# Performance work log

Measured on AMD Instinct MI355X. Metric: run time of the kernel, lower is better.

## Reference

```python
import jax, jax.numpy as jnp
import numpy as np

B, S, D = 4, 4096, 512
HEADS, NS, NEXT = 8, 32, 2048
HD = D // HEADS
SCALE = 1.0 / np.sqrt(HD)


def setup_inputs() -> dict:
    key = jax.random.key(0)
    ks = jax.random.split(key, 12)
    w_scale = 1.0 / np.sqrt(D)
    return {
        "sequence_tokens": jax.random.normal(ks[0], (B, S, D), jnp.float32),
        "sequence_mask": jnp.ones((B, S), dtype=bool),
        "ns_tokens": jax.random.normal(ks[1], (B, NS, D), jnp.float32),
        "ns_mask": jnp.ones((B, NS), dtype=bool),
        "next_sequence_length": NEXT,
        "Wq": jax.random.normal(ks[2], (D, D), jnp.float32) * w_scale,
        "Wk": jax.random.normal(ks[3], (D, D), jnp.float32) * w_scale,
        "Wv": jax.random.normal(ks[4], (D, D), jnp.float32) * w_scale,
        "ns_q_w": jax.random.normal(ks[5], (NS, D, D), jnp.float32) * w_scale,
        "ns_k_w": jax.random.normal(ks[6], (NS, D, D), jnp.float32) * w_scale,
        "ns_v_w": jax.random.normal(ks[7], (NS, D, D), jnp.float32) * w_scale,
        "Wo": jax.random.normal(ks[8], (D, D), jnp.float32) * w_scale,
    }


def reference(sequence_tokens, sequence_mask, ns_tokens, ns_mask,
              next_sequence_length, Wq, Wk, Wv, ns_q_w, ns_k_w, ns_v_w, Wo):
    b, s, d = sequence_tokens.shape
    ns = ns_tokens.shape[1]
    nxt = next_sequence_length

    seq_q = sequence_tokens[:, -nxt:]
    seq_q_mask = sequence_mask[:, -nxt:]

    # mixed projections: standard linear for seq tokens, per-position weights for NS tokens
    q = jnp.concatenate([seq_q @ Wq.T,
                         jnp.einsum('bnd,ndo->bno', ns_tokens, ns_q_w)], axis=1)
    k = jnp.concatenate([sequence_tokens @ Wk.T,
                         jnp.einsum('bnd,ndo->bno', ns_tokens, ns_k_w)], axis=1)
    v = jnp.concatenate([sequence_tokens @ Wv.T,
                         jnp.einsum('bnd,ndo->bno', ns_tokens, ns_v_w)], axis=1)

    def heads(x):  # [b, t, d] -> [b, h, t, hd]
        return x.reshape(b, -1, HEADS, HD).transpose(0, 2, 1, 3)
    q, k, v = heads(q), heads(k), heads(v)

    total = s + ns
    q_pos = jnp.concatenate([jnp.arange(s - nxt, s), jnp.arange(s, total)])
    k_pos = jnp.arange(total)
    causal = k_pos[None, :] <= q_pos[:, None]              # [Q, K]
    key_mask = jnp.concatenate([sequence_mask, ns_mask], axis=1)  # [b, K]

    logits = jnp.einsum('bhqd,bhkd->bhqk',
                        q.astype(jnp.float32), k.astype(jnp.float32)) * SCALE
    logits = jnp.where(causal[None, None], logits, -10000.0)
    logits = jnp.where(key_mask[:, None, None, :], logits, -10000.0)
    w = jax.nn.softmax(logits, axis=-1).astype(q.dtype)

    att = jnp.einsum('bhqk,bhkd->bhqd', w, v)
    att = att.transpose(0, 2, 1, 3).reshape(b, nxt + ns, d)
    att = att @ Wo.T

    seq_out = att[:, :nxt] * seq_q_mask[..., None].astype(att.dtype)
    ns_out = att[:, nxt:] * ns_mask[..., None].astype(att.dtype)
    return (seq_out, ns_out)
```

## Files before the change

### kernel.cpp

```cpp
#include <hip/hip_runtime.h>

#define NBATCH 4
#define SEQ    4096
#define DMODEL 512
#define NHEAD  8
#define HDIM   64
#define NSN    32
#define NXT    2048
#define QLEN   2080
#define KLEN   4128

using bf16x8 = __attribute__((ext_vector_type(8))) short;
using f32x4  = __attribute__((ext_vector_type(4))) float;

typedef __attribute__((address_space(1))) unsigned int gu32;
typedef __attribute__((address_space(3))) unsigned int lu32;

#define QSCALE 0.18033688f

__device__ __forceinline__ unsigned short f2bf(float f) {
  unsigned int u = __float_as_uint(f);
  u += 0x7FFF + ((u >> 16) & 1);
  return (unsigned short)(u >> 16);
}

__device__ __forceinline__ float bf2f(unsigned short u) {
  return __uint_as_float((unsigned int)u << 16);
}

__device__ __forceinline__ f32x4 mfma16(bf16x8 a, bf16x8 b, f32x4 c) {
  return __builtin_amdgcn_mfma_f32_16x16x32_bf16(a, b, c, 0, 0, 0);
}

__device__ __forceinline__ void gload_lds16(const void* g, void* lds_base) {
  __builtin_amdgcn_global_load_lds((const gu32*)g, (lu32*)lds_base, 16, 0, 0);
}

__device__ __forceinline__ unsigned int cvt_pk_bf16(float lo, float hi) {
  unsigned int r;
  asm("v_cvt_pk_bf16_f32 %0, %1, %2" : "=v"(r) : "v"(lo), "v"(hi));
  return r;
}

__global__ __launch_bounds__(256) void cvt_f32_bf16_v4(const float* __restrict__ src,
                                                       unsigned short* __restrict__ dst, int n4) {
  int i = blockIdx.x * 256 + threadIdx.x;
  if (i >= n4) return;
  float4 v = reinterpret_cast<const float4*>(src)[i];
  ushort4 r;
  r.x = f2bf(v.x); r.y = f2bf(v.y); r.z = f2bf(v.z); r.w = f2bf(v.w);
  reinterpret_cast<ushort4*>(dst)[i] = r;
}

__global__ __launch_bounds__(256) void cvt_w4(const float* __restrict__ a, const float* __restrict__ b,
                                              const float* __restrict__ c, const float* __restrict__ d,
                                              unsigned short* __restrict__ dst) {
  const float* s = blockIdx.y == 0 ? a : blockIdx.y == 1 ? b : blockIdx.y == 2 ? c : d;
  int i = blockIdx.x * 256 + threadIdx.x;
  float4 v = reinterpret_cast<const float4*>(s)[i];
  ushort4 r;
  r.x = f2bf(v.x); r.y = f2bf(v.y); r.z = f2bf(v.z); r.w = f2bf(v.w);
  reinterpret_cast<ushort4*>(dst)[(size_t)blockIdx.y * 65536 + i] = r;
}

__global__ __launch_bounds__(256) void proj_gemm(const unsigned short* __restrict__ X,
                                                 const unsigned short* __restrict__ W,
                                                 unsigned short* __restrict__ Out,
                                                 int rpb_shift, int row_off, int out_L, float scale) {
  __shared__ unsigned short As[64 * 32];
  __shared__ unsigned short Bs[128 * 32];
  const int tid = threadIdx.x;
  const int w = tid >> 6, l = tid & 63;
  const int lg = l >> 4, lr = l & 15;
  const int row0 = blockIdx.x * 64, col0 = blockIdx.y * 128;
  const int mask = (1 << rpb_shift) - 1;

  f32x4 acc[8];
#pragma unroll
  for (int n = 0; n < 8; ++n) acc[n] = (f32x4){0.f, 0.f, 0.f, 0.f};

  const int sra = tid >> 2;
  const int sca = (tid & 3) * 8;
  const int srb = w * 16 + (l >> 2);
  const int scb = (l & 3) * 8;
  const int gra = row0 + sra;
  const int xrow = ((gra >> rpb_shift) << 12) + row_off + (gra & mask);

  for (int k0 = 0; k0 < 512; k0 += 32) {
    const unsigned short* gpa = X + (size_t)xrow * 512 + k0 + sca;
    gload_lds16(gpa, (char*)As + w * 1024);
#pragma unroll
    for (int i = 0; i < 2; ++i) {
      const unsigned short* gpb = W + (size_t)(col0 + srb + i * 64) * 512 + k0 + scb;
      gload_lds16(gpb, (char*)Bs + i * 4096 + w * 1024);
    }
    __syncthreads();
    const bf16x8 avf = *(const bf16x8*)&As[(w * 16 + lr) * 32 + lg * 8];
#pragma unroll
    for (int n = 0; n < 8; ++n) {
      const bf16x8 bv = *(const bf16x8*)&Bs[(n * 16 + lr) * 32 + lg * 8];
      acc[n] = mfma16(avf, bv, acc[n]);
    }
    __syncthreads();
  }

  const int crow = row0 + w * 16 + lg * 4;
#pragma unroll
  for (int n = 0; n < 8; ++n) {
    const int ccol = col0 + n * 16 + lr;
    const int hh = ccol >> 6, dd = ccol & 63;
#pragma unroll
    for (int r = 0; r < 4; ++r) {
      int cr = crow + r;
      int bb = cr >> rpb_shift, ii = cr & mask;
      Out[(((size_t)bb * NHEAD + hh) * out_L + ii) * HDIM + dd] = f2bf(acc[n][r] * scale);
    }
  }
}

__global__ __launch_bounds__(256) void ns_proj(const float* __restrict__ nst,
                                               const float* __restrict__ Wnq, const float* __restrict__ Wnk,
                                               const float* __restrict__ Wnv,
                                               unsigned short* __restrict__ Qb, unsigned short* __restrict__ Kb,
                                               unsigned short* __restrict__ Vb) {
  const int oc = blockIdx.x, n = blockIdx.y, p = blockIdx.z;
  const float* W = p == 0 ? Wnq : p == 1 ? Wnk : Wnv;
  unsigned short* Out = p == 0 ? Qb : p == 1 ? Kb : Vb;
  const int out_L = p == 0 ? QLEN : KLEN;
  const int orow = p == 0 ? NXT + n : SEQ + n;
  const float scale = p == 0 ? QSCALE : 1.f;

  __shared__ float xs[NBATCH][DMODEL];
  __shared__ float red[NBATCH][128];
  const int tid = threadIdx.x;
  for (int idx = tid; idx < NBATCH * DMODEL; idx += 256)
    xs[idx >> 9][idx & 511] = nst[(size_t)((idx >> 9) * NSN + n) * DMODEL + (idx & 511)];
  __syncthreads();

  const int o = oc * 128 + (tid & 127);
  const int dh = tid >> 7;
  float a0 = 0.f, a1 = 0.f, a2 = 0.f, a3 = 0.f;
  const float* wp = W + (size_t)n * DMODEL * DMODEL + o;
#pragma unroll 8
  for (int d = dh * 256; d < dh * 256 + 256; ++d) {
    float wv = wp[(size_t)d * DMODEL];
    a0 += xs[0][d] * wv; a1 += xs[1][d] * wv; a2 += xs[2][d] * wv; a3 += xs[3][d] * wv;
  }
  if (dh == 1) { red[0][tid & 127] = a0; red[1][tid & 127] = a1; red[2][tid & 127] = a2; red[3][tid & 127] = a3; }
  __syncthreads();
  if (dh == 0) {
    a0 += red[0][tid & 127]; a1 += red[1][tid & 127]; a2 += red[2][tid & 127]; a3 += red[3][tid & 127];
    int hh = o >> 6, dd = o & 63;
    float v[4] = {a0, a1, a2, a3};
#pragma unroll
    for (int b = 0; b < NBATCH; ++b)
      Out[(((size_t)b * NHEAD + hh) * out_L + orow) * HDIM + dd] = f2bf(v[b] * scale);
  }
}

__global__ __launch_bounds__(256) void vtrans(const unsigned short* __restrict__ V,
                                              unsigned short* __restrict__ Vt) {
  __shared__ unsigned short t[64 * 64];
  const int tid = threadIdx.x;
  const int kv0 = blockIdx.x * 64, bh = blockIdx.y;
  const unsigned short* Vhp = V + (size_t)bh * KLEN * HDIM;
  unsigned short* Vtp = Vt + (size_t)bh * HDIM * KLEN;

#pragma unroll
  for (int i = 0; i < 2; ++i) {
    int c = i * 256 + tid;
    int row = c >> 3, c8 = c & 7;
    int kvg = kv0 + row; if (kvg > KLEN - 1) kvg = KLEN - 1;
    int4 v4 = *(const int4*)(Vhp + (size_t)kvg * HDIM + c8 * 8);
    *(int4*)&t[row * 64 + ((c8 ^ ((row >> 3) & 7)) * 8)] = v4;
  }
  __syncthreads();
#pragma unroll
  for (int i = 0; i < 2; ++i) {
    int c = i * 256 + tid;
    int d = c >> 3, k8 = c & 7;
    if (kv0 + k8 * 8 <= KLEN - 8) {
      unsigned int wd[4];
#pragma unroll
      for (int jj = 0; jj < 4; ++jj) {
        int ka = k8 * 8 + jj * 2, kb2 = ka + 1;
        unsigned int lo = t[ka  * 64 + (((d >> 3) ^ ((ka  >> 3) & 7)) * 8) + (d & 7)];
        unsigned int hi = t[kb2 * 64 + (((d >> 3) ^ ((kb2 >> 3) & 7)) * 8) + (d & 7)];
        wd[jj] = lo | (hi << 16);
      }
      int4 o; o.x = wd[0]; o.y = wd[1]; o.z = wd[2]; o.w = wd[3];
      *(int4*)(Vtp + (size_t)d * KLEN + kv0 + k8 * 8) = o;
    }
  }
}

__global__ __launch_bounds__(256) void attn_kernel(const unsigned short* __restrict__ Qb,
                                                   const unsigned short* __restrict__ Kb,
                                                   const unsigned short* __restrict__ Vtg,
                                                   unsigned short* __restrict__ PoA,
                                                   float* __restrict__ PlA,
                                                   unsigned short* __restrict__ PoB,
                                                   float* __restrict__ PlB) {
  __shared__ unsigned short Ks[64 * 64];
  __shared__ unsigned short Vs[64 * 64];

  const int tid = threadIdx.x;
  const int w = tid >> 6, l = tid & 63;
  const int lg = l >> 4, lr = l & 15;
  const bool geven = (l & 16) == 0;
  const int bx = (int)blockIdx.x;
  const int qb = 32 - bx / 3;
  const int sp = bx - 3 * (32 - qb);
  const int bh = (int)blockIdx.z * NHEAD + (int)blockIdx.y;
  const int q0 = qb * 64;
  const int base = NXT + q0;
  const int nkb = (base >> 6) + 1;
  const int t0 = (sp * nkb) / 3;
  const int t1 = ((sp + 1) * nkb) / 3;

  const unsigned short* Qh = Qb + (size_t)bh * QLEN * HDIM;
  const unsigned short* Kh = Kb + (size_t)bh * KLEN * HDIM;
  const unsigned short* Vh = Vtg + (size_t)bh * HDIM * KLEN;

  int qrow = q0 + w * 16 + lr; if (qrow > QLEN - 1) qrow = QLEN - 1;
  const bf16x8 qa0 = *(const bf16x8*)(Qh + (size_t)qrow * HDIM + lg * 8);
  const bf16x8 qa1 = *(const bf16x8*)(Qh + (size_t)qrow * HDIM + 32 + lg * 8);

  f32x4 acc[4];
#pragma unroll
  for (int n = 0; n < 4; ++n) acc[n] = (f32x4){0.f, 0.f, 0.f, 0.f};
  float lsum = 0.f;

  const bf16x8 ones = {(short)0x3F80, (short)0x3F80, (short)0x3F80, (short)0x3F80,
                       (short)0x3F80, (short)0x3F80, (short)0x3F80, (short)0x3F80};

  const int rloc = l >> 3;
  const int jsrc = ((l & 7) ^ rloc) * 8;

  for (int kb = t0; kb < t1; ++kb) {
    const int kv0 = kb * 64;
    if (kv0 + 64 <= KLEN) {
#pragma unroll
      for (int i = 0; i < 2; ++i) {
        const int r8 = (w * 2 + i) * 8;
        gload_lds16(Kh + (size_t)(kv0 + r8 + rloc) * HDIM + jsrc, &Ks[r8 * 64]);
        gload_lds16(Vh + (size_t)(r8 + rloc) * KLEN + kv0 + jsrc, &Vs[r8 * 64]);
      }
    } else {
#pragma unroll
      for (int i = 0; i < 2; ++i) {
        const int r8 = (w * 2 + i) * 8;
        int kr = kv0 + r8 + rloc; if (kr > KLEN - 1) kr = KLEN - 1;
        gload_lds16(Kh + (size_t)kr * HDIM + jsrc, &Ks[r8 * 64]);
        int vc = kv0 + jsrc; if (vc > KLEN - 8) vc = KLEN - 8;
        gload_lds16(Vh + (size_t)(r8 + rloc) * KLEN + vc, &Vs[r8 * 64]);
      }
    }
    __syncthreads();

    f32x4 s[4];
#pragma unroll
    for (int n = 0; n < 4; ++n) {
      const int rk = n * 16 + lr;
      const bf16x8 k0 = *(const bf16x8*)&Ks[rk * 64 + ((lg ^ (rk & 7)) * 8)];
      const bf16x8 k1 = *(const bf16x8*)&Ks[rk * 64 + (((4 + lg) ^ (rk & 7)) * 8)];
      s[n] = mfma16(k0, qa0, (f32x4){0.f, 0.f, 0.f, 0.f});
      s[n] = mfma16(k1, qa1, s[n]);
    }

    if (kb == nkb - 1) {
      const int qk_lim = base + w * 16 + lr;
#pragma unroll
      for (int n = 0; n < 4; ++n)
#pragma unroll
        for (int r = 0; r < 4; ++r)
          if (kv0 + n * 16 + lg * 4 + r > qk_lim) s[n][r] = -1e30f;
    }

#pragma unroll
    for (int n = 0; n < 4; ++n)
#pragma unroll
      for (int r = 0; r < 4; ++r) s[n][r] = exp2f(s[n][r]);

    unsigned int wpk[4][2];
#pragma unroll
    for (int n = 0; n < 4; ++n) {
      wpk[n][0] = cvt_pk_bf16(s[n][0], s[n][1]);
      wpk[n][1] = cvt_pk_bf16(s[n][2], s[n][3]);
    }
    bf16x8 pb[2];
#pragma unroll
    for (int ks = 0; ks < 2; ++ks) {
      unsigned int A0 = wpk[2 * ks][0], B0 = wpk[2 * ks + 1][0];
      unsigned int A1 = wpk[2 * ks][1], B1 = wpk[2 * ks + 1][1];
      asm("v_permlane32_swap_b32 %0, %1" : "+v"(A0), "+v"(B0));
      asm("v_permlane32_swap_b32 %0, %1" : "+v"(A1), "+v"(B1));
      unsigned int sA0 = __builtin_amdgcn_ds_swizzle(A0, 0x401F);
      unsigned int sA1 = __builtin_amdgcn_ds_swizzle(A1, 0x401F);
      unsigned int sB0 = __builtin_amdgcn_ds_swizzle(B0, 0x401F);
      unsigned int sB1 = __builtin_amdgcn_ds_swizzle(B1, 0x401F);
      int4 words;
      words.x = geven ? A0 : sB0;
      words.y = geven ? A1 : sB1;
      words.z = geven ? sA0 : B0;
      words.w = geven ? sA1 : B1;
      pb[ks] = *(bf16x8*)&words;
    }

    f32x4 acc_s = (f32x4){0.f, 0.f, 0.f, 0.f};
    acc_s = mfma16(ones, pb[0], acc_s);
    acc_s = mfma16(ones, pb[1], acc_s);
    lsum += acc_s[0];

#pragma unroll
    for (int n = 0; n < 4; ++n) {
      const int rv = n * 16 + lr;
#pragma unroll
      for (int ks = 0; ks < 2; ++ks) {
        const bf16x8 vv = *(const bf16x8*)&Vs[rv * 64 + (((ks * 4 + lg) ^ (rv & 7)) * 8)];
        acc[n] = mfma16(vv, pb[ks], acc[n]);
      }
    }

    __syncthreads();
  }

  const int qi = q0 + w * 16 + lr;
  if (qi < QLEN) {
    unsigned short* po; float* pl; size_t rowp;
    if (sp < 2) { rowp = (size_t)(sp * 32 + bh) * QLEN + qi; po = PoA + rowp * 64; pl = PlA + rowp; }
    else        { rowp = (size_t)bh * QLEN + qi;             po = PoB + rowp * 64; pl = PlB + rowp; }
#pragma unroll
    for (int n = 0; n < 4; ++n) {
      ushort4 pk;
      pk.x = f2bf(acc[n][0]); pk.y = f2bf(acc[n][1]);
      pk.z = f2bf(acc[n][2]); pk.w = f2bf(acc[n][3]);
      *(ushort4*)(po + n * 16 + lg * 4) = pk;
    }
    if (l < 16) *pl = lsum;
  }
}

__global__ __launch_bounds__(256) void attn_combine(const unsigned short* __restrict__ PoA,
                                                    const float* __restrict__ PlA,
                                                    const unsigned short* __restrict__ PoB,
                                                    const float* __restrict__ PlB,
                                                    unsigned short* __restrict__ Att) {
  const int bh = blockIdx.y;
  const int idx = blockIdx.x * 256 + threadIdx.x;
  const int qi = idx >> 3, dc = (idx & 7) * 8;
  const size_t row = (size_t)bh * QLEN + qi;
  const float l0 = PlA[row];
  const float l1 = PlA[(size_t)32 * QLEN + row];
  const float l2 = PlB[row];
  const float inv = 1.f / (l0 + l1 + l2);
  const bf16x8 o0 = *(const bf16x8*)(PoA + row * 64 + dc);
  const bf16x8 o1 = *(const bf16x8*)(PoA + ((size_t)32 * QLEN + row) * 64 + dc);
  const bf16x8 o2 = *(const bf16x8*)(PoB + row * 64 + dc);
  unsigned short out[8];
#pragma unroll
  for (int j = 0; j < 8; ++j)
    out[j] = f2bf((bf2f((unsigned short)o0[j]) + bf2f((unsigned short)o1[j]) +
                   bf2f((unsigned short)o2[j])) * inv);
  const int b = bh >> 3, h = bh & 7;
  *(int4*)(Att + ((size_t)b * QLEN + qi) * DMODEL + h * HDIM + dc) = *(int4*)out;
}

__global__ __launch_bounds__(256) void out_gemm(const unsigned short* __restrict__ A,
                                                const unsigned short* __restrict__ W,
                                                float* __restrict__ Out) {
  __shared__ unsigned short As[64 * 32];
  __shared__ unsigned short Bs[128 * 32];
  const int tid = threadIdx.x;
  const int w = tid >> 6, l = tid & 63;
  const int lg = l >> 4, lr = l & 15;
  const int row0 = blockIdx.x * 64, col0 = blockIdx.y * 128;

  f32x4 acc[8];
#pragma unroll
  for (int n = 0; n < 8; ++n) acc[n] = (f32x4){0.f, 0.f, 0.f, 0.f};

  const int sra = tid >> 2;
  const int sca = (tid & 3) * 8;
  const int srb = w * 16 + (l >> 2);
  const int scb = (l & 3) * 8;

  for (int k0 = 0; k0 < 512; k0 += 32) {
    const unsigned short* gpa = A + (size_t)(row0 + sra) * 512 + k0 + sca;
    gload_lds16(gpa, (char*)As + w * 1024);
#pragma unroll
    for (int i = 0; i < 2; ++i) {
      const unsigned short* gpb = W + (size_t)(col0 + srb + i * 64) * 512 + k0 + scb;
      gload_lds16(gpb, (char*)Bs + i * 4096 + w * 1024);
    }
    __syncthreads();
    const bf16x8 avf = *(const bf16x8*)&As[(w * 16 + lr) * 32 + lg * 8];
#pragma unroll
    for (int n = 0; n < 8; ++n) {
      const bf16x8 bv = *(const bf16x8*)&Bs[(n * 16 + lr) * 32 + lg * 8];
      acc[n] = mfma16(avf, bv, acc[n]);
    }
    __syncthreads();
  }

  const int crow = row0 + w * 16 + lg * 4;
#pragma unroll
  for (int n = 0; n < 8; ++n) {
    const int ccol = col0 + n * 16 + lr;
#pragma unroll
    for (int r = 0; r < 4; ++r) {
      int cr = crow + r;
      int bb = cr / QLEN, ii = cr - bb * QLEN;
      size_t off = ii < NXT
                     ? ((size_t)bb * NXT + ii) * DMODEL + ccol
                     : (size_t)NBATCH * NXT * DMODEL + ((size_t)bb * NSN + (ii - NXT)) * DMODEL + ccol;
      Out[off] = acc[n][r];
    }
  }
}

extern "C" void kernel_launch(void* const* d_in, const int* in_sizes, int n_in,
                              void* d_out, int out_size, void* d_ws, size_t ws_size,
                              hipStream_t stream) {
  const float* seq = (const float*)d_in[0];
  const float* nst = (const float*)d_in[2];
  const float* Wq  = (const float*)d_in[5];
  const float* Wk  = (const float*)d_in[6];
  const float* Wv  = (const float*)d_in[7];
  const float* nsq = (const float*)d_in[8];
  const float* nsk = (const float*)d_in[9];
  const float* nsv = (const float*)d_in[10];
  const float* Wo  = (const float*)d_in[11];
  float* out = (float*)d_out;

  char* ws = (char*)d_ws;
  unsigned short* Xbf  = (unsigned short*)(ws);
  unsigned short* Wqb  = (unsigned short*)(ws + 16777216);
  unsigned short* Wkb  = Wqb + 262144;
  unsigned short* Wvb  = Wkb + 262144;
  unsigned short* Wob  = Wvb + 262144;
  unsigned short* Qbuf = (unsigned short*)(ws + 18874368);
  unsigned short* Kbuf = (unsigned short*)(ws + 27394048);
  unsigned short* Vbuf = (unsigned short*)(ws + 44302336);
  unsigned short* Att  = (unsigned short*)(ws + 61210624);
  unsigned short* Vtg  = (unsigned short*)(ws + 69730304);
  unsigned short* PoA = (unsigned short*)(ws);
  float*          PlA = (float*)(ws + 17039360);
  unsigned short* PoB = (unsigned short*)(ws + 44302336);
  float*          PlB = (float*)(ws + 52822016);
  if (ws_size < 86638592) return;

  cvt_f32_bf16_v4<<<dim3(8192), dim3(256), 0, stream>>>(seq, Xbf, 2097152);
  cvt_w4<<<dim3(256, 4), dim3(256), 0, stream>>>(Wq, Wk, Wv, Wo, Wqb);
  proj_gemm<<<dim3(256, 4), dim3(256), 0, stream>>>(Xbf, Wkb, Kbuf, 12, 0, KLEN, 1.f);
  proj_gemm<<<dim3(256, 4), dim3(256), 0, stream>>>(Xbf, Wvb, Vbuf, 12, 0, KLEN, 1.f);
  proj_gemm<<<dim3(128, 4), dim3(256), 0, stream>>>(Xbf, Wqb, Qbuf, 11, 2048, QLEN, QSCALE);
  ns_proj<<<dim3(4, 32, 3), dim3(256), 0, stream>>>(nst, nsq, nsk, nsv, Qbuf, Kbuf, Vbuf);
  vtrans<<<dim3(65, 32), dim3(256), 0, stream>>>(Vbuf, Vtg);
  attn_kernel<<<dim3(99, 8, 4), dim3(256), 0, stream>>>(Qbuf, Kbuf, Vtg, PoA, PlA, PoB, PlB);
  attn_combine<<<dim3(65, 32), dim3(256), 0, stream>>>(PoA, PlA, PoB, PlB, Att);
  out_gemm<<<dim3(130, 4), dim3(256), 0, stream>>>(Att, Wob, out);
}
```

Measured before the change: 220.2 us.

## Write V projection directly in transposed layout and drop vtrans kernel

Adds a proj_gemm_vt kernel that stores V projection output straight into the head-major transposed [b,h,d,k] layout used by attention. The separate vtrans kernel launch and its extra read and write pass over V are removed. ns_proj also writes its V rows transposed and is split across 4 K-chunks with 64 outputs per block, doubling its grid. The transposed stores are 8-byte ushort4 writes strided by KLEN, so they coalesce less well than the original row-major stores.

```diff
diff --git a/kernel.cpp b/kernel.cpp
--- a/kernel.cpp
+++ b/kernel.cpp
@@ -118,78 +118,107 @@
   }
 }
 
+__global__ __launch_bounds__(256) void proj_gemm_vt(const unsigned short* __restrict__ X,
+                                                    const unsigned short* __restrict__ W,
+                                                    unsigned short* __restrict__ Vt) {
+  __shared__ unsigned short As[64 * 32];
+  __shared__ unsigned short Bs[128 * 32];
+  const int tid = threadIdx.x;
+  const int w = tid >> 6, l = tid & 63;
+  const int lg = l >> 4, lr = l & 15;
+  const int row0 = blockIdx.x * 64, col0 = blockIdx.y * 128;
+
+  f32x4 acc[8];
+#pragma unroll
+  for (int n = 0; n < 8; ++n) acc[n] = (f32x4){0.f, 0.f, 0.f, 0.f};
+
+  const int sra = tid >> 2;
+  const int sca = (tid & 3) * 8;
+  const int srb = w * 16 + (l >> 2);
+  const int scb = (l & 3) * 8;
+  const int xrow = row0 + sra;
+
+  for (int k0 = 0; k0 < 512; k0 += 32) {
+    const unsigned short* gpa = X + (size_t)xrow * 512 + k0 + sca;
+    gload_lds16(gpa, (char*)As + w * 1024);
+#pragma unroll
+    for (int i = 0; i < 2; ++i) {
+      const unsigned short* gpb = W + (size_t)(col0 + srb + i * 64) * 512 + k0 + scb;
+      gload_lds16(gpb, (char*)Bs + i * 4096 + w * 1024);
+    }
+    __syncthreads();
+    const bf16x8 avf = *(const bf16x8*)&As[(w * 16 + lr) * 32 + lg * 8];
+#pragma unroll
+    for (int n = 0; n < 8; ++n) {
+      const bf16x8 bv = *(const bf16x8*)&Bs[(n * 16 + lr) * 32 + lg * 8];
+      acc[n] = mfma16(avf, bv, acc[n]);
+    }
+    __syncthreads();
+  }
+
+  const int crow = row0 + w * 16 + lg * 4;
+  const int bb = crow >> 12, ii = crow & 4095;
+#pragma unroll
+  for (int n = 0; n < 8; ++n) {
+    const int ccol = col0 + n * 16 + lr;
+    const int hh = ccol >> 6, dd = ccol & 63;
+    ushort4 pk;
+    pk.x = f2bf(acc[n][0]); pk.y = f2bf(acc[n][1]);
+    pk.z = f2bf(acc[n][2]); pk.w = f2bf(acc[n][3]);
+    *(ushort4*)(Vt + ((size_t)(bb * NHEAD + hh) * HDIM + dd) * KLEN + ii) = pk;
+  }
+}
+
 __global__ __launch_bounds__(256) void ns_proj(const float* __restrict__ nst,
                                                const float* __restrict__ Wnq, const float* __restrict__ Wnk,
                                                const float* __restrict__ Wnv,
                                                unsigned short* __restrict__ Qb, unsigned short* __restrict__ Kb,
-                                               unsigned short* __restrict__ Vb) {
+                                               unsigned short* __restrict__ Vt) {
   const int oc = blockIdx.x, n = blockIdx.y, p = blockIdx.z;
   const float* W = p == 0 ? Wnq : p == 1 ? Wnk : Wnv;
-  unsigned short* Out = p == 0 ? Qb : p == 1 ? Kb : Vb;
-  const int out_L = p == 0 ? QLEN : KLEN;
-  const int orow = p == 0 ? NXT + n : SEQ + n;
   const float scale = p == 0 ? QSCALE : 1.f;
 
   __shared__ float xs[NBATCH][DMODEL];
-  __shared__ float red[NBATCH][128];
+  __shared__ float red[3][NBATCH][64];
   const int tid = threadIdx.x;
   for (int idx = tid; idx < NBATCH * DMODEL; idx += 256)
     xs[idx >> 9][idx & 511] = nst[(size_t)((idx >> 9) * NSN + n) * DMODEL + (idx & 511)];
   __syncthreads();
 
-  const int o = oc * 128 + (tid & 127);
-  const int dh = tid >> 7;
+  const int o = oc * 64 + (tid & 63);
+  const int dh = tid >> 6;
   float a0 = 0.f, a1 = 0.f, a2 = 0.f, a3 = 0.f;
   const float* wp = W + (size_t)n * DMODEL * DMODEL + o;
 #pragma unroll 8
-  for (int d = dh * 256; d < dh * 256 + 256; ++d) {
+  for (int d = dh * 128; d < dh * 128 + 128; ++d) {
     float wv = wp[(size_t)d * DMODEL];
     a0 += xs[0][d] * wv; a1 += xs[1][d] * wv; a2 += xs[2][d] * wv; a3 += xs[3][d] * wv;
   }
-  if (dh == 1) { red[0][tid & 127] = a0; red[1][tid & 127] = a1; red[2][tid & 127] = a2; red[3][tid & 127] = a3; }
+  if (dh) {
+    red[dh - 1][0][tid & 63] = a0; red[dh - 1][1][tid & 63] = a1;
+    red[dh - 1][2][tid & 63] = a2; red[dh - 1][3][tid & 63] = a3;
+  }
   __syncthreads();
   if (dh == 0) {
-    a0 += red[0][tid & 127]; a1 += red[1][tid & 127]; a2 += red[2][tid & 127]; a3 += red[3][tid & 127];
-    int hh = o >> 6, dd = o & 63;
+#pragma unroll
+    for (int j = 0; j < 3; ++j) {
+      a0 += red[j][0][tid & 63]; a1 += red[j][1][tid & 63];
+      a2 += red[j][2][tid & 63]; a3 += red[j][3][tid & 63];
+    }
+    const int hh = o >> 6, dd = o & 63;
     float v[4] = {a0, a1, a2, a3};
-#pragma unroll
-    for (int b = 0; b < NBATCH; ++b)
-      Out[(((size_t)b * NHEAD + hh) * out_L + orow) * HDIM + dd] = f2bf(v[b] * scale);
-  }
-}
-
-__global__ __launch_bounds__(256) void vtrans(const unsigned short* __restrict__ V,
-                                              unsigned short* __restrict__ Vt) {
-  __shared__ unsigned short t[64 * 64];
-  const int tid = threadIdx.x;
-  const int kv0 = blockIdx.x * 64, bh = blockIdx.y;
-  const unsigned short* Vhp = V + (size_t)bh * KLEN * HDIM;
-  unsigned short* Vtp = Vt + (size_t)bh * HDIM * KLEN;
-
-#pragma unroll
-  for (int i = 0; i < 2; ++i) {
-    int c = i * 256 + tid;
-    int row = c >> 3, c8 = c & 7;
-    int kvg = kv0 + row; if (kvg > KLEN - 1) kvg = KLEN - 1;
-    int4 v4 = *(const int4*)(Vhp + (size_t)kvg * HDIM + c8 * 8);
-    *(int4*)&t[row * 64 + ((c8 ^ ((row >> 3) & 7)) * 8)] = v4;
-  }
-  __syncthreads();
-#pragma unroll
-  for (int i = 0; i < 2; ++i) {
-    int c = i * 256 + tid;
-    int d = c >> 3, k8 = c & 7;
-    if (kv0 + k8 * 8 <= KLEN - 8) {
-      unsigned int wd[4];
-#pragma unroll
-      for (int jj = 0; jj < 4; ++jj) {
-        int ka = k8 * 8 + jj * 2, kb2 = ka + 1;
-        unsigned int lo = t[ka  * 64 + (((d >> 3) ^ ((ka  >> 3) & 7)) * 8) + (d & 7)];
-        unsigned int hi = t[kb2 * 64 + (((d >> 3) ^ ((kb2 >> 3) & 7)) * 8) + (d & 7)];
-        wd[jj] = lo | (hi << 16);
-      }
-      int4 o; o.x = wd[0]; o.y = wd[1]; o.z = wd[2]; o.w = wd[3];
-      *(int4*)(Vtp + (size_t)d * KLEN + kv0 + k8 * 8) = o;
+    if (p == 2) {
+      const int orow = SEQ + n;
+#pragma unroll
+      for (int b = 0; b < NBATCH; ++b)
+        Vt[((size_t)(b * NHEAD + hh) * HDIM + dd) * KLEN + orow] = f2bf(v[b]);
+    } else {
+      unsigned short* Out = p == 0 ? Qb : Kb;
+      const int out_L = p == 0 ? QLEN : KLEN;
+      const int orow  = p == 0 ? NXT + n : SEQ + n;
+#pragma unroll
+      for (int b = 0; b < NBATCH; ++b)
+        Out[(((size_t)b * NHEAD + hh) * out_L + orow) * HDIM + dd] = f2bf(v[b] * scale);
     }
   }
 }
@@ -441,7 +470,6 @@
   unsigned short* Wob  = Wvb + 262144;
   unsigned short* Qbuf = (unsigned short*)(ws + 18874368);
   unsigned short* Kbuf = (unsigned short*)(ws + 27394048);
-  unsigned short* Vbuf = (unsigned short*)(ws + 44302336);
   unsigned short* Att  = (unsigned short*)(ws + 61210624);
   unsigned short* Vtg  = (unsigned short*)(ws + 69730304);
   unsigned short* PoA = (unsigned short*)(ws);
@@ -453,10 +481,9 @@
   cvt_f32_bf16_v4<<<dim3(8192), dim3(256), 0, stream>>>(seq, Xbf, 2097152);
   cvt_w4<<<dim3(256, 4), dim3(256), 0, stream>>>(Wq, Wk, Wv, Wo, Wqb);
   proj_gemm<<<dim3(256, 4), dim3(256), 0, stream>>>(Xbf, Wkb, Kbuf, 12, 0, KLEN, 1.f);
-  proj_gemm<<<dim3(256, 4), dim3(256), 0, stream>>>(Xbf, Wvb, Vbuf, 12, 0, KLEN, 1.f);
+  proj_gemm_vt<<<dim3(256, 4), dim3(256), 0, stream>>>(Xbf, Wvb, Vtg);
   proj_gemm<<<dim3(128, 4), dim3(256), 0, stream>>>(Xbf, Wqb, Qbuf, 11, 2048, QLEN, QSCALE);
-  ns_proj<<<dim3(4, 32, 3), dim3(256), 0, stream>>>(nst, nsq, nsk, nsv, Qbuf, Kbuf, Vbuf);
-  vtrans<<<dim3(65, 32), dim3(256), 0, stream>>>(Vbuf, Vtg);
+  ns_proj<<<dim3(8, 32, 3), dim3(256), 0, stream>>>(nst, nsq, nsk, nsv, Qbuf, Kbuf, Vtg);
   attn_kernel<<<dim3(99, 8, 4), dim3(256), 0, stream>>>(Qbuf, Kbuf, Vtg, PoA, PlA, PoB, PlB);
   attn_combine<<<dim3(65, 32), dim3(256), 0, stream>>>(PoA, PlA, PoB, PlB, Att);
   out_gemm<<<dim3(130, 4), dim3(256), 0, stream>>>(Att, Wob, out);
```

Result: faster. 214.1 us (-2.8%).
